# Optimization experiments

Measured on AMD Instinct MI355X. Metric: run time of the kernel, lower is better.

The kernel has to match this reference:

```python
import jax, jax.numpy as jnp
import numpy as np

B, N, K = 64, 1024, 16  # graphs per batch, nodes per graph, top-k (k=16 hardcoded in module)
EPS = 1e-20


def setup_inputs() -> dict:
    key = jax.random.key(0)
    ks = jax.random.split(key, 6)
    C = 128
    x = jax.random.normal(ks[0], (B * N, C), jnp.float32)
    pos = jax.random.normal(ks[1], (B * N, 3), jnp.float32)
    W1 = jax.random.normal(ks[2], (C, C), jnp.float32) / np.sqrt(C).astype(np.float32)
    b1 = jnp.zeros((C,), jnp.float32)
    gamma = jnp.ones((C,), jnp.float32)
    beta = jnp.zeros((C,), jnp.float32)
    W2 = jax.random.normal(ks[3], (C, 10), jnp.float32) / np.sqrt(C).astype(np.float32)
    b2 = jnp.zeros((10,), jnp.float32)
    t = jnp.ones((1,), jnp.float32)
    return dict(x=x, pos=pos, W1=W1, b1=b1, gamma=gamma, beta=beta, W2=W2, b2=b2, t=t)


def _edge_arrays(idx):
    # idx: (B, N, K) per-target top-k source node indices (graph-local)
    offs = (jnp.arange(B, dtype=jnp.int32) * N)[:, None, None]
    src = (idx + offs).reshape(-1)
    tgt = (jnp.broadcast_to(jnp.arange(N, dtype=jnp.int32)[None, :, None], (B, N, K)) + offs).reshape(-1)
    return jnp.stack([src, tgt])  # (2, B*N*K)


def _knn_edges(pos):
    # KNNGraph(k=16) on positions, loop=False (exclude self)
    p = pos.reshape(B, N, 3)
    d2 = jnp.sum((p[:, :, None, :] - p[:, None, :, :]) ** 2, axis=-1)  # (B,N,N)
    d2 = d2 + jnp.eye(N, dtype=d2.dtype) * 1e10
    _, idx = jax.lax.top_k(-d2, K)  # nearest K per node
    return _edge_arrays(idx)


def reference(x, pos, W1, b1, gamma, beta, W2, b2, t):
    key = jax.random.key(42)
    k1, k2 = jax.random.split(key)
    # tg MLP: lin -> batchnorm -> relu -> lin (training-mode batch stats over nodes)
    h = x @ W1 + b1
    mu = h.mean(axis=0)
    var = h.var(axis=0)
    h = (h - mu) / jnp.sqrt(var + 1e-5) * gamma + beta
    h = jax.nn.relu(h)
    emb = h @ W2 + b2  # (B*N, 10)
    emb = emb + jax.random.uniform(k1, emb.shape, emb.dtype) * 0.001
    e = emb.reshape(B, N, 10)
    # pairwise distances per graph (vectorized over the python loop in the original)
    diff = e[:, :, None, :] - e[:, None, :, :]  # (B,N,N,10)
    dist = jnp.linalg.norm(diff, axis=-1)  # (B,N,N)
    p = jnp.exp(-t[0] * dist ** 2)
    u = jax.random.uniform(k2, p.shape, p.dtype)
    gumbel = -jnp.log(-jnp.log(u + EPS) + EPS)
    noisy_logits = jnp.log(p + EPS) + gumbel
    # torch topk over dim=0 (sources) for each target column -> transpose then top_k on last axis
    vals, idx = jax.lax.top_k(jnp.swapaxes(noisy_logits, 1, 2), K)  # (B,N,K)
    vals = jax.nn.softmax(vals, axis=-1)
    vals = vals / vals.max(axis=-1, keepdims=True)
    soft_idx = _edge_arrays(idx)  # (2, B*N*K)
    knn_idx = _knn_edges(pos)
    edge_index = jnp.concatenate([soft_idx, knn_idx], axis=1)
    return vals.reshape(-1), soft_idx, edge_index
```

## Files before the change

kernel.cpp:

```cpp
#include <hip/hip_runtime.h>
#include <stdint.h>
#include <math.h>

#define BG 64
#define NG 1024
#define KK 16
#define CC 128
#define NNODE (BG * NG)
#define NSOFT (BG * NG * KK)
#define FEPS 1e-20f

__host__ __device__ __forceinline__ uint32_t rotl32u(uint32_t x, int r) {
  return (x << r) | (x >> (32 - r));
}

__host__ __device__ __forceinline__ void tf2x32(uint32_t k0, uint32_t k1,
                                                uint32_t x0, uint32_t x1,
                                                uint32_t &o0, uint32_t &o1) {
  uint32_t k2 = k0 ^ k1 ^ 0x1BD11BDAu;
  x0 += k0; x1 += k1;
#define TFR(r) { x0 += x1; x1 = rotl32u(x1, r); x1 ^= x0; }
  TFR(13) TFR(15) TFR(26) TFR(6)
  x0 += k1; x1 += k2 + 1u;
  TFR(17) TFR(29) TFR(16) TFR(24)
  x0 += k2; x1 += k0 + 2u;
  TFR(13) TFR(15) TFR(26) TFR(6)
  x0 += k0; x1 += k1 + 3u;
  TFR(17) TFR(29) TFR(16) TFR(24)
  x0 += k1; x1 += k2 + 4u;
  TFR(13) TFR(15) TFR(26) TFR(6)
  x0 += k2; x1 += k0 + 5u;
#undef TFR
  o0 = x0; o1 = x1;
}

__device__ __forceinline__ float jax_uniform01(uint32_t ka, uint32_t kb, uint32_t m) {
  uint32_t o0, o1;
  tf2x32(ka, kb, 0u, m, o0, o1);
  uint32_t bits = o0 ^ o1;
  float f = __uint_as_float((bits >> 9) | 0x3f800000u) - 1.0f;
  return fmaxf(f, 0.0f);
}

__device__ __forceinline__ int vbin_soft(float v) {
  float fb = (v + 50.0f) * (256.0f / 67.0f);
  fb = fminf(fmaxf(fb, 0.0f), 255.0f);
  return (int)fb;
}
__device__ __forceinline__ int vbin_knn(float v) {
  float fb = (v + 64.0f) * 4.0f;
  fb = fminf(fmaxf(fb, 0.0f), 255.0f);
  return (int)fb;
}

#define LDS_WAIT() asm volatile("s_waitcnt lgkmcnt(0)" ::: "memory")

__global__ __launch_bounds__(256) void k_gemm1(const float* __restrict__ x,
                                               const float* __restrict__ W1,
                                               const float* __restrict__ b1,
                                               float* __restrict__ h,
                                               float* __restrict__ p1,
                                               float* __restrict__ p2) {
  __shared__ __align__(16) float xs[64 * 128];
  const int t = threadIdx.x;
  const size_t blockBase = (size_t)blockIdx.x * (64 * 128);
  #pragma unroll
  for (int j = 0; j < 32; ++j) xs[t + j * 256] = x[blockBase + t + j * 256];
  __syncthreads();
  const int c = t & 127;
  const int rg = t >> 7;
  float acc[32];
  #pragma unroll
  for (int j = 0; j < 32; ++j) acc[j] = 0.f;
  const float* xrow = &xs[rg * 32 * 128];
  for (int k4 = 0; k4 < 128; k4 += 4) {
    const float w0 = W1[(size_t)(k4 + 0) * 128 + c];
    const float w1 = W1[(size_t)(k4 + 1) * 128 + c];
    const float w2 = W1[(size_t)(k4 + 2) * 128 + c];
    const float w3 = W1[(size_t)(k4 + 3) * 128 + c];
    #pragma unroll
    for (int j = 0; j < 32; ++j) {
      const float4 xv = *(const float4*)&xrow[j * 128 + k4];
      acc[j] = fmaf(xv.x, w0, acc[j]);
      acc[j] = fmaf(xv.y, w1, acc[j]);
      acc[j] = fmaf(xv.z, w2, acc[j]);
      acc[j] = fmaf(xv.w, w3, acc[j]);
    }
  }
  const float bb = b1[c];
  float s1 = 0.f, s2 = 0.f;
  #pragma unroll
  for (int j = 0; j < 32; ++j) {
    const float v = acc[j] + bb;
    h[blockBase + (size_t)(rg * 32 + j) * 128 + c] = v;
    s1 += v;
    s2 = fmaf(v, v, s2);
  }
  __syncthreads();
  float* r1 = xs;
  float* r2 = xs + 256;
  r1[rg * 128 + c] = s1;
  r2[rg * 128 + c] = s2;
  __syncthreads();
  if (t < 128) {
    p1[(size_t)t * 1024 + blockIdx.x] = r1[t] + r1[128 + t];
  } else {
    const int cc = t - 128;
    p2[(size_t)cc * 1024 + blockIdx.x] = r2[cc] + r2[128 + cc];
  }
}

__global__ __launch_bounds__(256) void k_bn_final(const float* __restrict__ p1,
                                                  const float* __restrict__ p2,
                                                  const float* __restrict__ gamma,
                                                  const float* __restrict__ beta,
                                                  float* __restrict__ scale,
                                                  float* __restrict__ shift) {
  const int c = blockIdx.x, t = threadIdx.x;
  const float* q1 = p1 + (size_t)c * 1024;
  const float* q2 = p2 + (size_t)c * 1024;
  float a1 = q1[t] + q1[t + 256] + q1[t + 512] + q1[t + 768];
  float a2 = q2[t] + q2[t + 256] + q2[t + 512] + q2[t + 768];
  __shared__ float r1[256], r2[256];
  r1[t] = a1; r2[t] = a2;
  __syncthreads();
  for (int o = 128; o > 0; o >>= 1) {
    if (t < o) { r1[t] += r1[t + o]; r2[t] += r2[t + o]; }
    __syncthreads();
  }
  if (t == 0) {
    const float mu = r1[0] * (1.0f / NNODE);
    float var = r2[0] * (1.0f / NNODE) - mu * mu;
    var = fmaxf(var, 0.f);
    const float sc = gamma[c] / sqrtf(var + 1e-5f);
    scale[c] = sc;
    shift[c] = beta[c] - mu * sc;
  }
}

__global__ __launch_bounds__(256) void k_emb(const float* __restrict__ h,
                                             const float* __restrict__ scale,
                                             const float* __restrict__ shift,
                                             const float* __restrict__ W2,
                                             const float* __restrict__ b2,
                                             float* __restrict__ e,
                                             uint32_t ka, uint32_t kb) {
  __shared__ __align__(16) float hn[64 * 132];
  const int t = threadIdx.x;
  const int rowBase = blockIdx.x * 64;
  {
    const int c = t & 127;
    const float sc = scale[c], sh = shift[c];
    #pragma unroll
    for (int j = 0; j < 32; ++j) {
      const int r = (t >> 7) + j * 2;
      const float v = fmaf(h[(size_t)(rowBase + r) * 128 + c], sc, sh);
      hn[r * 132 + c] = fmaxf(v, 0.f);
    }
  }
  __syncthreads();
  #pragma unroll
  for (int j = 0; j < 3; ++j) {
    const int o = t + j * 256;
    if (o < 640) {
      const int r = o / 10;
      const int col = o - r * 10;
      float acc = 0.f;
      for (int k4 = 0; k4 < 128; k4 += 4) {
        const float4 hv = *(const float4*)&hn[r * 132 + k4];
        acc = fmaf(hv.x, W2[(k4 + 0) * 10 + col], acc);
        acc = fmaf(hv.y, W2[(k4 + 1) * 10 + col], acc);
        acc = fmaf(hv.z, W2[(k4 + 2) * 10 + col], acc);
        acc = fmaf(hv.w, W2[(k4 + 3) * 10 + col], acc);
      }
      acc += b2[col];
      const uint32_t m = (uint32_t)(rowBase + r) * 10u + (uint32_t)col;
      const float u = jax_uniform01(ka, kb, m);
      e[(size_t)(rowBase + r) * 10 + col] = acc + u * 0.001f;
    }
  }
}

__global__ __launch_bounds__(512, 4) void k_soft(const float* __restrict__ e,
                                                 const float* __restrict__ tsc,
                                                 float* __restrict__ out,
                                                 uint32_t ka, uint32_t kb) {
  __shared__ __align__(16) float2 els2[5 * NG];
  __shared__ uint32_t bins[8][256];
  __shared__ float    cv[8][48];
  __shared__ int      cidx[8][48];
  __shared__ uint32_t cnt[8];
  __shared__ float    o16v[8][16];
  __shared__ int      o16i[8][16];

  const int t = threadIdx.x, lane = t & 63, w = t >> 6;
  const int node = blockIdx.x * 8 + w;
  const int b = blockIdx.x >> 7;
  const int jt = node & (NG - 1);
  const float negt = -tsc[0];
  const float* eg = e + (size_t)b * (NG * 10);

  { uint4 z = {0, 0, 0, 0}; *(uint4*)&bins[w][lane * 4] = z; }
  if (lane == 0) cnt[w] = 0u;

  for (int s = t; s < NG; s += 512) {
    const float2* rp = (const float2*)(eg + (size_t)s * 10);
    els2[0 * NG + s] = rp[0];
    els2[1 * NG + s] = rp[1];
    els2[2 * NG + s] = rp[2];
    els2[3 * NG + s] = rp[3];
    els2[4 * NG + s] = rp[4];
  }
  __syncthreads();

  float ej[10];
  #pragma unroll
  for (int p = 0; p < 5; ++p) {
    const float2 a = els2[p * NG + jt];
    ej[2 * p] = a.x; ej[2 * p + 1] = a.y;
  }

  float vv[16];
  const uint32_t mL = ((uint32_t)b << 20) + ((uint32_t)lane << 10) + (uint32_t)jt;
  const uint32_t kxa = ka, kxb = kb;
  const uint32_t kxc = ka ^ kb ^ 0x1BD11BDAu;

#define DIST(ACC, S) { \
    const float2 r0 = els2[0 * NG + (S)]; \
    const float2 r1 = els2[1 * NG + (S)]; \
    const float2 r2 = els2[2 * NG + (S)]; \
    const float2 r3 = els2[3 * NG + (S)]; \
    const float2 r4 = els2[4 * NG + (S)]; \
    float dd; \
    dd = ej[0] - r0.x; ACC = dd * dd; \
    dd = ej[1] - r0.y; ACC = fmaf(dd, dd, ACC); \
    dd = ej[2] - r1.x; ACC = fmaf(dd, dd, ACC); \
    dd = ej[3] - r1.y; ACC = fmaf(dd, dd, ACC); \
    dd = ej[4] - r2.x; ACC = fmaf(dd, dd, ACC); \
    dd = ej[5] - r2.y; ACC = fmaf(dd, dd, ACC); \
    dd = ej[6] - r3.x; ACC = fmaf(dd, dd, ACC); \
    dd = ej[7] - r3.y; ACC = fmaf(dd, dd, ACC); \
    dd = ej[8] - r4.x; ACC = fmaf(dd, dd, ACC); \
    dd = ej[9] - r4.y; ACC = fmaf(dd, dd, ACC); }

#define TFR4(r) { \
    xA0 += xA1; xA1 = rotl32u(xA1, r); xA1 ^= xA0; \
    xB0 += xB1; xB1 = rotl32u(xB1, r); xB1 ^= xB0; \
    xC0 += xC1; xC1 = rotl32u(xC1, r); xC1 ^= xC0; \
    xD0 += xD1; xD1 = rotl32u(xD1, r); xD1 ^= xD0; }
#define INJ4(A, B) { \
    xA0 += (A); xA1 += (B); \
    xB0 += (A); xB1 += (B); \
    xC0 += (A); xC1 += (B); \
    xD0 += (A); xD1 += (B); }

#define TAIL(ACC, X0, X1, ST) { \
    const uint32_t bits = (X0) ^ (X1); \
    float uu = __uint_as_float((bits >> 9) | 0x3f800000u) - 1.0f; \
    uu = fmaxf(uu, 0.0f); \
    const float dist = sqrtf(ACC); \
    const float d2 = dist * dist; \
    const float p = __expf(negt * d2); \
    const float li = __logf(uu + FEPS); \
    const float g = -__logf(FEPS - li); \
    const float v = __logf(p + FEPS) + g; \
    vv[ST] = v; \
    atomicAdd(&bins[w][vbin_soft(v)], 1u); }

  #pragma unroll
  for (int g4 = 0; g4 < 4; ++g4) {
    const int sA = (g4 * 4 + 0) * 64 + lane;
    const int sB = (g4 * 4 + 1) * 64 + lane;
    const int sC = (g4 * 4 + 2) * 64 + lane;
    const int sD = (g4 * 4 + 3) * 64 + lane;
    float aA, aB, aC, aD;
    DIST(aA, sA)
    DIST(aB, sB)
    DIST(aC, sC)
    DIST(aD, sD)
    uint32_t xA0 = kxa, xA1 = (mL + (uint32_t)((g4 * 4 + 0) << 16)) + kxb;
    uint32_t xB0 = kxa, xB1 = (mL + (uint32_t)((g4 * 4 + 1) << 16)) + kxb;
    uint32_t xC0 = kxa, xC1 = (mL + (uint32_t)((g4 * 4 + 2) << 16)) + kxb;
    uint32_t xD0 = kxa, xD1 = (mL + (uint32_t)((g4 * 4 + 3) << 16)) + kxb;
    TFR4(13) TFR4(15) TFR4(26) TFR4(6)
    INJ4(kxb, kxc + 1u)
    TFR4(17) TFR4(29) TFR4(16) TFR4(24)
    INJ4(kxc, kxa + 2u)
    TFR4(13) TFR4(15) TFR4(26) TFR4(6)
    INJ4(kxa, kxb + 3u)
    TFR4(17) TFR4(29) TFR4(16) TFR4(24)
    INJ4(kxb, kxc + 4u)
    TFR4(13) TFR4(15) TFR4(26) TFR4(6)
    INJ4(kxc, kxa + 5u)
    TAIL(aA, xA0, xA1, g4 * 4 + 0)
    TAIL(aB, xB0, xB1, g4 * 4 + 1)
    TAIL(aC, xC0, xC1, g4 * 4 + 2)
    TAIL(aD, xD0, xD1, g4 * 4 + 3)
  }
#undef DIST
#undef TFR4
#undef INJ4
#undef TAIL
  LDS_WAIT();

  const uint4 c4 = *(const uint4*)&bins[w][lane * 4];
  const uint32_t lsum = c4.x + c4.y + c4.z + c4.w;
  uint32_t xs = lsum;
  #pragma unroll
  for (int off = 1; off < 64; off <<= 1) {
    uint32_t tt = (uint32_t)__shfl_down((int)xs, off, 64);
    if (lane + off < 64) xs += tt;
  }
  const uint32_t after = xs - lsum;
  const uint32_t s3 = c4.w + after;
  const uint32_t s2 = c4.z + s3;
  const uint32_t s1 = c4.y + s2;
  const uint32_t s0 = c4.x + s1;
  int localB = -1;
  if (s3 >= 16u) localB = lane * 4 + 3;
  else if (s2 >= 16u) localB = lane * 4 + 2;
  else if (s1 >= 16u) localB = lane * 4 + 1;
  else if (s0 >= 16u) localB = lane * 4 + 0;
  const unsigned long long msk = __ballot(localB >= 0);
  const int hl = 63 - __builtin_clzll(msk);
  const int B = __shfl(localB, hl, 64);

  #pragma unroll
  for (int st = 0; st < 16; ++st) {
    if (vbin_soft(vv[st]) >= B) {
      const uint32_t pos = atomicAdd(&cnt[w], 1u);
      if (pos < 48u) { cv[w][pos] = vv[st]; cidx[w][pos] = st * 64 + lane; }
    }
  }
  LDS_WAIT();

  int C = (int)cnt[w]; if (C > 48) C = 48;
  const float mvv = (lane < C) ? cv[w][lane] : 0.f;
  const int   mii = (lane < C) ? cidx[w][lane] : 0;
  int rank = 0;
  for (int j = 0; j < C; ++j) {
    const float vj = cv[w][j];
    const int ij = cidx[w][j];
    if (vj > mvv || (vj == mvv && ij < mii)) ++rank;
  }
  if (lane < C && rank < 16) { o16v[w][rank] = mvv; o16i[w][rank] = mii; }
  LDS_WAIT();

  if (lane < 16) {
    const float vq = o16v[w][lane];
    const float m0 = o16v[w][0];
    float uex = __expf(vq - m0);
    float ss = uex;
    #pragma unroll
    for (int off = 1; off < 16; off <<= 1) ss += __shfl_xor(ss, off, 16);
    const float u0 = __shfl(uex, 0, 16);
    const float s0v = u0 / ss;
    const float sv = uex / ss;
    const float o = sv / s0v;
    const size_t base = (size_t)node * KK + lane;
    const float tgtf = (float)node;
    const float srcf = (float)(b * NG + o16i[w][lane]);
    out[base] = o;
    out[(size_t)NSOFT + base] = srcf;
    out[2 * (size_t)NSOFT + base] = tgtf;
    out[3 * (size_t)NSOFT + base] = srcf;
    out[5 * (size_t)NSOFT + base] = tgtf;
  }
}

__global__ __launch_bounds__(512) void k_knn(const float* __restrict__ pos,
                                             float* __restrict__ out) {
  __shared__ float    pls[3 * NG];
  __shared__ uint32_t bins[8][256];
  __shared__ float    cv[8][48];
  __shared__ int      cidx[8][48];
  __shared__ uint32_t cnt[8];
  __shared__ int      o16i[8][16];

  const int t = threadIdx.x, lane = t & 63, w = t >> 6;
  const int node = blockIdx.x * 8 + w;
  const int b = blockIdx.x >> 7;
  const int it = node & (NG - 1);
  const float* pg = pos + (size_t)b * (NG * 3);

  { uint4 z = {0, 0, 0, 0}; *(uint4*)&bins[w][lane * 4] = z; }
  if (lane == 0) cnt[w] = 0u;

  for (int s = t; s < NG; s += 512) {
    pls[0 * NG + s] = pg[(size_t)s * 3 + 0];
    pls[1 * NG + s] = pg[(size_t)s * 3 + 1];
    pls[2 * NG + s] = pg[(size_t)s * 3 + 2];
  }
  __syncthreads();

  const float px = pls[0 * NG + it];
  const float py = pls[1 * NG + it];
  const float pz = pls[2 * NG + it];

  float vv[16];
  #pragma unroll
  for (int st = 0; st < 16; ++st) {
    const int s = st * 64 + lane;
    const float dx = px - pls[0 * NG + s];
    const float dy = py - pls[1 * NG + s];
    const float dz = pz - pls[2 * NG + s];
    float d2 = dx * dx;
    d2 = fmaf(dy, dy, d2);
    d2 = fmaf(dz, dz, d2);
    if (s == it) d2 += 1e10f;
    const float v = -d2;
    vv[st] = v;
    atomicAdd(&bins[w][vbin_knn(v)], 1u);
  }
  LDS_WAIT();

  const uint4 c4 = *(const uint4*)&bins[w][lane * 4];
  const uint32_t lsum = c4.x + c4.y + c4.z + c4.w;
  uint32_t xs = lsum;
  #pragma unroll
  for (int off = 1; off < 64; off <<= 1) {
    uint32_t tt = (uint32_t)__shfl_down((int)xs, off, 64);
    if (lane + off < 64) xs += tt;
  }
  const uint32_t after = xs - lsum;
  const uint32_t s3 = c4.w + after;
  const uint32_t s2 = c4.z + s3;
  const uint32_t s1 = c4.y + s2;
  const uint32_t s0 = c4.x + s1;
  int localB = -1;
  if (s3 >= 16u) localB = lane * 4 + 3;
  else if (s2 >= 16u) localB = lane * 4 + 2;
  else if (s1 >= 16u) localB = lane * 4 + 1;
  else if (s0 >= 16u) localB = lane * 4 + 0;
  const unsigned long long msk = __ballot(localB >= 0);
  const int hl = 63 - __builtin_clzll(msk);
  const int B = __shfl(localB, hl, 64);

  #pragma unroll
  for (int st = 0; st < 16; ++st) {
    if (vbin_knn(vv[st]) >= B) {
      const uint32_t pos = atomicAdd(&cnt[w], 1u);
      if (pos < 48u) { cv[w][pos] = vv[st]; cidx[w][pos] = st * 64 + lane; }
    }
  }
  LDS_WAIT();

  int C = (int)cnt[w]; if (C > 48) C = 48;
  const float mvv = (lane < C) ? cv[w][lane] : 0.f;
  const int   mii = (lane < C) ? cidx[w][lane] : 0;
  int rank = 0;
  for (int j = 0; j < C; ++j) {
    const float vj = cv[w][j];
    const int ij = cidx[w][j];
    if (vj > mvv || (vj == mvv && ij < mii)) ++rank;
  }
  if (lane < C && rank < 16) o16i[w][rank] = mii;
  LDS_WAIT();

  if (lane < 16) {
    const size_t base = (size_t)node * KK + lane;
    out[4 * (size_t)NSOFT + base] = (float)(b * NG + o16i[w][lane]);
    out[6 * (size_t)NSOFT + base] = (float)node;
  }
}

extern "C" void kernel_launch(void* const* d_in, const int* in_sizes, int n_in,
                              void* d_out, int out_size, void* d_ws, size_t ws_size,
                              hipStream_t stream) {
  const float* x     = (const float*)d_in[0];
  const float* pos   = (const float*)d_in[1];
  const float* W1    = (const float*)d_in[2];
  const float* b1    = (const float*)d_in[3];
  const float* gamma = (const float*)d_in[4];
  const float* beta  = (const float*)d_in[5];
  const float* W2    = (const float*)d_in[6];
  const float* b2    = (const float*)d_in[7];
  const float* t     = (const float*)d_in[8];
  float* out = (float*)d_out;

  float* ws    = (float*)d_ws;
  float* h     = ws;
  float* e     = h + (size_t)NNODE * CC;
  float* p1    = e + (size_t)NNODE * 10;
  float* p2    = p1 + 128 * 1024;
  float* scale = p2 + 128 * 1024;
  float* shift = scale + CC;

  uint32_t k1a, k1b, k2a, k2b;
  tf2x32(0u, 42u, 0u, 0u, k1a, k1b);
  tf2x32(0u, 42u, 0u, 1u, k2a, k2b);

  k_gemm1<<<dim3(NNODE / 64), dim3(256), 0, stream>>>(x, W1, b1, h, p1, p2);
  k_bn_final<<<dim3(CC), dim3(256), 0, stream>>>(p1, p2, gamma, beta, scale, shift);
  k_emb<<<dim3(NNODE / 64), dim3(256), 0, stream>>>(h, scale, shift, W2, b2, e, k1a, k1b);
  k_knn<<<dim3(NNODE / 8), dim3(512), 0, stream>>>(pos, out);
  k_soft<<<dim3(NNODE / 8), dim3(512), 0, stream>>>(e, t, out, k2a, k2b);
}
```

Before: 424.4 us.

## Write embeddings in plane-major float2 layout and read soft sources via global/L1

k_emb now writes the 10-dim embeddings transposed into five float2 planes, with each node's pair contiguous within a plane. k_soft no longer stages the whole graph's embeddings into 40KB of LDS and skips the block-wide barrier. It reads source embeddings directly from global memory through the caches and drops the min-occupancy launch bound. It also caches each candidate's bin index in registers instead of recomputing it. The goal is higher occupancy and no staging copy, at the cost of many more global/L1 loads in the inner distance loop.

Result: slower. 468.1 us (+10.3%).

```diff
diff --git a/kernel.cpp b/kernel.cpp
--- a/kernel.cpp
+++ b/kernel.cpp
@@ -143,9 +143,10 @@
                                              const float* __restrict__ shift,
                                              const float* __restrict__ W2,
                                              const float* __restrict__ b2,
-                                             float* __restrict__ e,
+                                             float2* __restrict__ et2,
                                              uint32_t ka, uint32_t kb) {
   __shared__ __align__(16) float hn[64 * 132];
+  __shared__ float et[64 * 10];
   const int t = threadIdx.x;
   const int rowBase = blockIdx.x * 64;
   {
@@ -176,16 +177,21 @@
       acc += b2[col];
       const uint32_t m = (uint32_t)(rowBase + r) * 10u + (uint32_t)col;
       const float u = jax_uniform01(ka, kb, m);
-      e[(size_t)(rowBase + r) * 10 + col] = acc + u * 0.001f;
+      et[r * 10 + col] = acc + u * 0.001f;
     }
   }
-}
-
-__global__ __launch_bounds__(512, 4) void k_soft(const float* __restrict__ e,
-                                                 const float* __restrict__ tsc,
-                                                 float* __restrict__ out,
-                                                 uint32_t ka, uint32_t kb) {
-  __shared__ __align__(16) float2 els2[5 * NG];
+  __syncthreads();
+  if (t < 320) {
+    const int r = t & 63, p = t >> 6;
+    et2[(size_t)p * NNODE + rowBase + r] =
+        make_float2(et[r * 10 + 2 * p], et[r * 10 + 2 * p + 1]);
+  }
+}
+
+__global__ __launch_bounds__(512) void k_soft(const float2* __restrict__ et2,
+                                              const float* __restrict__ tsc,
+                                              float* __restrict__ out,
+                                              uint32_t ka, uint32_t kb) {
   __shared__ uint32_t bins[8][256];
   __shared__ float    cv[8][48];
   __shared__ int      cidx[8][48];
@@ -195,42 +201,34 @@
 
   const int t = threadIdx.x, lane = t & 63, w = t >> 6;
   const int node = blockIdx.x * 8 + w;
-  const int b = blockIdx.x >> 7;
+  const int b = node >> 10;
   const int jt = node & (NG - 1);
+  const int gb = b << 10;
   const float negt = -tsc[0];
-  const float* eg = e + (size_t)b * (NG * 10);
 
   { uint4 z = {0, 0, 0, 0}; *(uint4*)&bins[w][lane * 4] = z; }
   if (lane == 0) cnt[w] = 0u;
-
-  for (int s = t; s < NG; s += 512) {
-    const float2* rp = (const float2*)(eg + (size_t)s * 10);
-    els2[0 * NG + s] = rp[0];
-    els2[1 * NG + s] = rp[1];
-    els2[2 * NG + s] = rp[2];
-    els2[3 * NG + s] = rp[3];
-    els2[4 * NG + s] = rp[4];
-  }
-  __syncthreads();
+  LDS_WAIT();
 
   float ej[10];
   #pragma unroll
   for (int p = 0; p < 5; ++p) {
-    const float2 a = els2[p * NG + jt];
+    const float2 a = et2[(size_t)p * NNODE + node];
     ej[2 * p] = a.x; ej[2 * p + 1] = a.y;
   }
 
   float vv[16];
+  int   vb[16];
   const uint32_t mL = ((uint32_t)b << 20) + ((uint32_t)lane << 10) + (uint32_t)jt;
   const uint32_t kxa = ka, kxb = kb;
   const uint32_t kxc = ka ^ kb ^ 0x1BD11BDAu;
 
 #define DIST(ACC, S) { \
-    const float2 r0 = els2[0 * NG + (S)]; \
-    const float2 r1 = els2[1 * NG + (S)]; \
-    const float2 r2 = els2[2 * NG + (S)]; \
-    const float2 r3 = els2[3 * NG + (S)]; \
-    const float2 r4 = els2[4 * NG + (S)]; \
+    const float2 r0 = et2[0 * (size_t)NNODE + gb + (S)]; \
+    const float2 r1 = et2[1 * (size_t)NNODE + gb + (S)]; \
+    const float2 r2 = et2[2 * (size_t)NNODE + gb + (S)]; \
+    const float2 r3 = et2[3 * (size_t)NNODE + gb + (S)]; \
+    const float2 r4 = et2[4 * (size_t)NNODE + gb + (S)]; \
     float dd; \
     dd = ej[0] - r0.x; ACC = dd * dd; \
     dd = ej[1] - r0.y; ACC = fmaf(dd, dd, ACC); \
@@ -264,8 +262,9 @@
     const float li = __logf(uu + FEPS); \
     const float g = -__logf(FEPS - li); \
     const float v = __logf(p + FEPS) + g; \
-    vv[ST] = v; \
-    atomicAdd(&bins[w][vbin_soft(v)], 1u); }
+    const int bn = vbin_soft(v); \
+    vv[ST] = v; vb[ST] = bn; \
+    atomicAdd(&bins[w][bn], 1u); }
 
   #pragma unroll
   for (int g4 = 0; g4 < 4; ++g4) {
@@ -327,7 +326,7 @@
 
   #pragma unroll
   for (int st = 0; st < 16; ++st) {
-    if (vbin_soft(vv[st]) >= B) {
+    if (vb[st] >= B) {
       const uint32_t pos = atomicAdd(&cnt[w], 1u);
       if (pos < 48u) { cv[w][pos] = vv[st]; cidx[w][pos] = st * 64 + lane; }
     }
@@ -359,7 +358,7 @@
     const float o = sv / s0v;
     const size_t base = (size_t)node * KK + lane;
     const float tgtf = (float)node;
-    const float srcf = (float)(b * NG + o16i[w][lane]);
+    const float srcf = (float)(gb + o16i[w][lane]);
     out[base] = o;
     out[(size_t)NSOFT + base] = srcf;
     out[2 * (size_t)NSOFT + base] = tgtf;
@@ -379,7 +378,7 @@
 
   const int t = threadIdx.x, lane = t & 63, w = t >> 6;
   const int node = blockIdx.x * 8 + w;
-  const int b = blockIdx.x >> 7;
+  const int b = node >> 10;
   const int it = node & (NG - 1);
   const float* pg = pos + (size_t)b * (NG * 3);
 
@@ -480,8 +479,8 @@
 
   float* ws    = (float*)d_ws;
   float* h     = ws;
-  float* e     = h + (size_t)NNODE * CC;
-  float* p1    = e + (size_t)NNODE * 10;
+  float2* et2  = (float2*)(h + (size_t)NNODE * CC);
+  float* p1    = (float*)(et2 + 5 * (size_t)NNODE);
   float* p2    = p1 + 128 * 1024;
   float* scale = p2 + 128 * 1024;
   float* shift = scale + CC;
@@ -492,7 +491,7 @@
 
   k_gemm1<<<dim3(NNODE / 64), dim3(256), 0, stream>>>(x, W1, b1, h, p1, p2);
   k_bn_final<<<dim3(CC), dim3(256), 0, stream>>>(p1, p2, gamma, beta, scale, shift);
-  k_emb<<<dim3(NNODE / 64), dim3(256), 0, stream>>>(h, scale, shift, W2, b2, e, k1a, k1b);
+  k_emb<<<dim3(NNODE / 64), dim3(256), 0, stream>>>(h, scale, shift, W2, b2, et2, k1a, k1b);
   k_knn<<<dim3(NNODE / 8), dim3(512), 0, stream>>>(pos, out);
-  k_soft<<<dim3(NNODE / 8), dim3(512), 0, stream>>>(e, t, out, k2a, k2b);
-}
+  k_soft<<<dim3(NNODE / 8), dim3(512), 0, stream>>>(et2, t, out, k2a, k2b);
+}
```

## Replace LDS histogram threshold with ballot-based bisection for top-k selection

Applied to the files above, without the earlier changes.

In both the soft and knn top-k kernels, the per-wave 256-bin LDS histogram (atomic increments plus a prefix scan) is replaced by a bisection search on the threshold value. Each step counts the candidates above the midpoint using ballot and popcount across the 16 register values. This removes the LDS atomics and the shared histogram storage, which lowers LDS use and can raise occupancy; the launch-bounds occupancy hint on k_soft is also dropped. In exchange it runs 24–26 serial iterations of 16 ballots each, and a fixed search range that misses the actual values could select too few or too many candidates, overflowing the 48-entry candidate buffer.

Measured after the change: 486.2 us. 1.15x slower.

```diff
diff --git a/kernel.cpp b/kernel.cpp
--- a/kernel.cpp
+++ b/kernel.cpp
@@ -40,17 +40,6 @@
   uint32_t bits = o0 ^ o1;
   float f = __uint_as_float((bits >> 9) | 0x3f800000u) - 1.0f;
   return fmaxf(f, 0.0f);
-}
-
-__device__ __forceinline__ int vbin_soft(float v) {
-  float fb = (v + 50.0f) * (256.0f / 67.0f);
-  fb = fminf(fmaxf(fb, 0.0f), 255.0f);
-  return (int)fb;
-}
-__device__ __forceinline__ int vbin_knn(float v) {
-  float fb = (v + 64.0f) * 4.0f;
-  fb = fminf(fmaxf(fb, 0.0f), 255.0f);
-  return (int)fb;
 }
 
 #define LDS_WAIT() asm volatile("s_waitcnt lgkmcnt(0)" ::: "memory")
@@ -181,12 +170,11 @@
   }
 }
 
-__global__ __launch_bounds__(512, 4) void k_soft(const float* __restrict__ e,
-                                                 const float* __restrict__ tsc,
-                                                 float* __restrict__ out,
-                                                 uint32_t ka, uint32_t kb) {
+__global__ __launch_bounds__(512) void k_soft(const float* __restrict__ e,
+                                              const float* __restrict__ tsc,
+                                              float* __restrict__ out,
+                                              uint32_t ka, uint32_t kb) {
   __shared__ __align__(16) float2 els2[5 * NG];
-  __shared__ uint32_t bins[8][256];
   __shared__ float    cv[8][48];
   __shared__ int      cidx[8][48];
   __shared__ uint32_t cnt[8];
@@ -200,7 +188,6 @@
   const float negt = -tsc[0];
   const float* eg = e + (size_t)b * (NG * 10);
 
-  { uint4 z = {0, 0, 0, 0}; *(uint4*)&bins[w][lane * 4] = z; }
   if (lane == 0) cnt[w] = 0u;
 
   for (int s = t; s < NG; s += 512) {
@@ -263,9 +250,7 @@
     const float p = __expf(negt * d2); \
     const float li = __logf(uu + FEPS); \
     const float g = -__logf(FEPS - li); \
-    const float v = __logf(p + FEPS) + g; \
-    vv[ST] = v; \
-    atomicAdd(&bins[w][vbin_soft(v)], 1u); }
+    vv[ST] = __logf(p + FEPS) + g; }
 
   #pragma unroll
   for (int g4 = 0; g4 < 4; ++g4) {
@@ -301,33 +286,22 @@
 #undef TFR4
 #undef INJ4
 #undef TAIL
-  LDS_WAIT();
-
-  const uint4 c4 = *(const uint4*)&bins[w][lane * 4];
-  const uint32_t lsum = c4.x + c4.y + c4.z + c4.w;
-  uint32_t xs = lsum;
-  #pragma unroll
-  for (int off = 1; off < 64; off <<= 1) {
-    uint32_t tt = (uint32_t)__shfl_down((int)xs, off, 64);
-    if (lane + off < 64) xs += tt;
-  }
-  const uint32_t after = xs - lsum;
-  const uint32_t s3 = c4.w + after;
-  const uint32_t s2 = c4.z + s3;
-  const uint32_t s1 = c4.y + s2;
-  const uint32_t s0 = c4.x + s1;
-  int localB = -1;
-  if (s3 >= 16u) localB = lane * 4 + 3;
-  else if (s2 >= 16u) localB = lane * 4 + 2;
-  else if (s1 >= 16u) localB = lane * 4 + 1;
-  else if (s0 >= 16u) localB = lane * 4 + 0;
-  const unsigned long long msk = __ballot(localB >= 0);
-  const int hl = 63 - __builtin_clzll(msk);
-  const int B = __shfl(localB, hl, 64);
+
+  float lo = -51.0f, hi = 17.0f;
+  #pragma unroll 1
+  for (int it = 0; it < 24; ++it) {
+    const float mid = 0.5f * (lo + hi);
+    int c = 0;
+    #pragma unroll
+    for (int st = 0; st < 16; ++st)
+      c += (int)__popcll(__ballot(vv[st] >= mid));
+    if (c >= 16) lo = mid; else hi = mid;
+  }
+  const float tau = lo;
 
   #pragma unroll
   for (int st = 0; st < 16; ++st) {
-    if (vbin_soft(vv[st]) >= B) {
+    if (vv[st] >= tau) {
       const uint32_t pos = atomicAdd(&cnt[w], 1u);
       if (pos < 48u) { cv[w][pos] = vv[st]; cidx[w][pos] = st * 64 + lane; }
     }
@@ -371,7 +345,6 @@
 __global__ __launch_bounds__(512) void k_knn(const float* __restrict__ pos,
                                              float* __restrict__ out) {
   __shared__ float    pls[3 * NG];
-  __shared__ uint32_t bins[8][256];
   __shared__ float    cv[8][48];
   __shared__ int      cidx[8][48];
   __shared__ uint32_t cnt[8];
@@ -383,7 +356,6 @@
   const int it = node & (NG - 1);
   const float* pg = pos + (size_t)b * (NG * 3);
 
-  { uint4 z = {0, 0, 0, 0}; *(uint4*)&bins[w][lane * 4] = z; }
   if (lane == 0) cnt[w] = 0u;
 
   for (int s = t; s < NG; s += 512) {
@@ -408,37 +380,24 @@
     d2 = fmaf(dy, dy, d2);
     d2 = fmaf(dz, dz, d2);
     if (s == it) d2 += 1e10f;
-    const float v = -d2;
-    vv[st] = v;
-    atomicAdd(&bins[w][vbin_knn(v)], 1u);
-  }
-  LDS_WAIT();
-
-  const uint4 c4 = *(const uint4*)&bins[w][lane * 4];
-  const uint32_t lsum = c4.x + c4.y + c4.z + c4.w;
-  uint32_t xs = lsum;
-  #pragma unroll
-  for (int off = 1; off < 64; off <<= 1) {
-    uint32_t tt = (uint32_t)__shfl_down((int)xs, off, 64);
-    if (lane + off < 64) xs += tt;
-  }
-  const uint32_t after = xs - lsum;
-  const uint32_t s3 = c4.w + after;
-  const uint32_t s2 = c4.z + s3;
-  const uint32_t s1 = c4.y + s2;
-  const uint32_t s0 = c4.x + s1;
-  int localB = -1;
-  if (s3 >= 16u) localB = lane * 4 + 3;
-  else if (s2 >= 16u) localB = lane * 4 + 2;
-  else if (s1 >= 16u) localB = lane * 4 + 1;
-  else if (s0 >= 16u) localB = lane * 4 + 0;
-  const unsigned long long msk = __ballot(localB >= 0);
-  const int hl = 63 - __builtin_clzll(msk);
-  const int B = __shfl(localB, hl, 64);
+    vv[st] = -d2;
+  }
+
+  float lo = -70.0f, hi = 1.0f;
+  #pragma unroll 1
+  for (int bs = 0; bs < 26; ++bs) {
+    const float mid = 0.5f * (lo + hi);
+    int c = 0;
+    #pragma unroll
+    for (int st = 0; st < 16; ++st)
+      c += (int)__popcll(__ballot(vv[st] >= mid));
+    if (c >= 16) lo = mid; else hi = mid;
+  }
+  const float tau = lo;
 
   #pragma unroll
   for (int st = 0; st < 16; ++st) {
-    if (vbin_knn(vv[st]) >= B) {
+    if (vv[st] >= tau) {
       const uint32_t pos = atomicAdd(&cnt[w], 1u);
       if (pos < 48u) { cv[w][pos] = vv[st]; cidx[w][pos] = st * 64 + lane; }
     }
```
